# Performance work log

Hardware: AMD Instinct MI355X
Metric: run time of the kernel (lower is better)

Reference implementation:

```python
import jax, jax.numpy as jnp
import numpy as np

D_MODEL = 512
D_INNER = 2 * D_MODEL          # Mamba expand=2
D_STATE = 16                   # Mamba default d_state
D_CONV = 4                     # Mamba default d_conv
DT_RANK = D_MODEL // 16        # ceil(512/16) = 32
B, L = 2, 2048


def setup_inputs() -> dict:
    key = jax.random.key(0)
    ks = jax.random.split(key, 12)
    s = 0.02
    return {
        "query": jax.random.normal(ks[0], (B, L, D_MODEL), jnp.float32),
        "value": jax.random.normal(ks[1], (B, L, D_MODEL), jnp.float32),
        "diff_ts": jax.random.normal(ks[2], (B, D_MODEL), jnp.float32),
        # AdaLN modulation: SiLU -> Linear(D, 2D) (random instead of zero-init to exercise math)
        "ada_w": jax.random.normal(ks[3], (2 * D_MODEL, D_MODEL), jnp.float32) * s,
        "ada_b": jax.random.normal(ks[4], (2 * D_MODEL,), jnp.float32) * s,
        # Mamba params
        "in_proj_w": jax.random.normal(ks[5], (2 * D_INNER, D_MODEL), jnp.float32) * s,
        "conv_w": jax.random.normal(ks[6], (D_INNER, D_CONV), jnp.float32) * 0.1,
        "conv_b": jax.random.normal(ks[7], (D_INNER,), jnp.float32) * 0.1,
        "x_proj_w": jax.random.normal(ks[8], (DT_RANK + 2 * D_STATE, D_INNER), jnp.float32) * s,
        "dt_proj_w": jax.random.normal(ks[9], (D_INNER, DT_RANK), jnp.float32) * 0.1,
        "dt_proj_b": jax.random.normal(ks[10], (D_INNER,), jnp.float32) * 0.1,
        "A_log": jnp.broadcast_to(jnp.log(jnp.arange(1, D_STATE + 1, dtype=jnp.float32)), (D_INNER, D_STATE)) * jnp.ones((D_INNER, 1), jnp.float32),
        "D_param": jnp.ones((D_INNER,), jnp.float32),
        "out_proj_w": jax.random.normal(ks[11], (D_MODEL, D_INNER), jnp.float32) * s,
        "ln_g": jnp.ones((D_MODEL,), jnp.float32),
        "ln_b": jnp.zeros((D_MODEL,), jnp.float32),
    }


def reference(query, value, diff_ts, ada_w, ada_b, in_proj_w, conv_w, conv_b,
              x_proj_w, dt_proj_w, dt_proj_b, A_log, D_param, out_proj_w, ln_g, ln_b):
    silu = jax.nn.silu
    # ---- AdaLN modulation of query ----
    m = silu(diff_ts) @ ada_w.T + ada_b            # (B, 2D)
    scale, shift = jnp.split(m, 2, axis=-1)        # (B, D) each
    x = query * (1.0 + scale[:, None, :]) + shift[:, None, :]

    # ---- Mamba block ----
    xz = x @ in_proj_w.T                           # (B, L, 2*d_inner)
    xm, z = jnp.split(xz, 2, axis=-1)
    # causal depthwise conv1d (kernel D_CONV)
    xp = jnp.pad(xm, ((0, 0), (D_CONV - 1, 0), (0, 0)))
    Lq = xm.shape[1]
    xc = sum(xp[:, k:k + Lq, :] * conv_w[:, k] for k in range(D_CONV)) + conv_b
    xc = silu(xc)                                  # (B, L, d_inner)

    xdb = xc @ x_proj_w.T                          # (B, L, dt_rank + 2*N)
    dt = xdb[..., :DT_RANK]
    Bm = xdb[..., DT_RANK:DT_RANK + D_STATE]       # (B, L, N)
    Cm = xdb[..., DT_RANK + D_STATE:]              # (B, L, N)
    delta = jax.nn.softplus(dt @ dt_proj_w.T + dt_proj_b)  # (B, L, d_inner)
    A = -jnp.exp(A_log)                            # (d_inner, N)

    # ---- selective scan: h_t = exp(dt*A) h_{t-1} + dt*B_t*x_t ; y_t = C_t . h_t ----
    def step(h, inp):
        d_t, x_t, B_t, C_t = inp                   # (B,d), (B,d), (B,N), (B,N)
        dA = jnp.exp(d_t[..., None] * A)           # (B, d, N)
        h = dA * h + (d_t * x_t)[..., None] * B_t[:, None, :]
        y = jnp.einsum('bdn,bn->bd', h, C_t)
        return h, y

    seq = (delta.transpose(1, 0, 2), xc.transpose(1, 0, 2),
           Bm.transpose(1, 0, 2), Cm.transpose(1, 0, 2))
    h0 = jnp.zeros((query.shape[0], D_INNER, D_STATE), delta.dtype)
    _, ys = jax.lax.scan(step, h0, seq)            # (L, B, d_inner)

    y = ys.transpose(1, 0, 2) + xc * D_param
    y = y * silu(z)
    attn = y @ out_proj_w.T                        # (B, L, D)

    # ---- residual (dropout p=0) + LayerNorm ----
    out = query + attn
    mu = out.mean(-1, keepdims=True)
    var = out.var(-1, keepdims=True)
    return (out - mu) / jnp.sqrt(var + 1e-5) * ln_g + ln_b
```

## Files before the change

kernel.cpp:

```cpp
#include <hip/hip_runtime.h>
#include <hip/hip_bf16.h>

#define D_MODEL 512
#define D_INNER 1024
#define D_STATE 16
#define DT_RANK 32
#define BB 2
#define LL 2048
#define RR (BB*LL)
#define NC 128
#define CS 16

typedef __attribute__((ext_vector_type(8))) short short8;
typedef __attribute__((ext_vector_type(4))) short short4v;
typedef __attribute__((ext_vector_type(4))) float f32x4;

static __device__ __forceinline__ short f2bf(float f) {
  union { __hip_bfloat16 h; short s; } u;
  u.h = __float2bfloat16(f);
  return u.s;
}
static __device__ __forceinline__ float bfs2f(short s) {
  union { short s; __hip_bfloat16 h; } u;
  u.s = s;
  return __bfloat162float(u.h);
}

static __device__ __forceinline__ void gload16(const short* gp, short* lp) {
  __builtin_amdgcn_global_load_lds((const __attribute__((address_space(1))) short*)gp,
                                   (__attribute__((address_space(3))) short*)lp,
                                   16, 0, 0);
}

__global__ void k_ada_cvtw(const float* __restrict__ diff,
                           const float* __restrict__ aw,
                           const float* __restrict__ ab,
                           float* __restrict__ m,
                           const float* __restrict__ inw,
                           const float* __restrict__ outw,
                           const float* __restrict__ xw,
                           short* __restrict__ inwb,
                           short* __restrict__ outwb,
                           short* __restrict__ xwb) {
  const int bx = blockIdx.x;
  const int t = threadIdx.x;
  if (bx < 8) {
    __shared__ float sd[D_MODEL];
    const int b = bx >> 2;
    const int jb = bx & 3;
    for (int k = t; k < D_MODEL; k += 256) {
      float v = diff[b*D_MODEL + k];
      sd[k] = v / (1.f + __expf(-v));
    }
    __syncthreads();
    const int j = jb*256 + t;
    const float4* wr = reinterpret_cast<const float4*>(aw + (size_t)j*D_MODEL);
    float acc = ab[j];
    #pragma unroll 4
    for (int k4 = 0; k4 < D_MODEL/4; ++k4) {
      float4 wv = wr[k4];
      acc += sd[4*k4]*wv.x + sd[4*k4+1]*wv.y + sd[4*k4+2]*wv.z + sd[4*k4+3]*wv.w;
    }
    m[b*(2*D_MODEL) + j] = acc;
  } else {
    const int N1 = 2048*512, N2 = 512*1024, N3 = 64*1024;
    const int idx = ((bx - 8)*256 + t)*4;
    if (idx < N1) {
      float4 v = *reinterpret_cast<const float4*>(inw + idx);
      short4v s = {f2bf(v.x), f2bf(v.y), f2bf(v.z), f2bf(v.w)};
      *reinterpret_cast<short4v*>(inwb + idx) = s;
    } else if (idx < N1 + N2) {
      float4 v = *reinterpret_cast<const float4*>(outw + (idx - N1));
      short4v s = {f2bf(v.x), f2bf(v.y), f2bf(v.z), f2bf(v.w)};
      *reinterpret_cast<short4v*>(outwb + (idx - N1)) = s;
    } else if (idx < N1 + N2 + N3) {
      float4 v = *reinterpret_cast<const float4*>(xw + (idx - N1 - N2));
      short4v s = {f2bf(v.x), f2bf(v.y), f2bf(v.z), f2bf(v.w)};
      *reinterpret_cast<short4v*>(xwb + (idx - N1 - N2)) = s;
    }
  }
}

__global__ void k_amod(const float* __restrict__ q,
                       const float* __restrict__ m,
                       short* __restrict__ amod,
                       float* __restrict__ xdb) {
  const int bx = blockIdx.x;
  const int t = threadIdx.x;
  const int NB = (RR*D_MODEL)/(256*4);
  if (bx < NB) {
    const int idx = (bx*256 + t)*4;
    const int r = idx >> 9, k = idx & 511;
    const float* mrow = m + (r >> 11)*(2*D_MODEL);
    float4 a = *reinterpret_cast<const float4*>(q + idx);
    float4 s = *reinterpret_cast<const float4*>(mrow + k);
    float4 h = *reinterpret_cast<const float4*>(mrow + D_MODEL + k);
    short4v o = {f2bf(a.x*(1.f+s.x)+h.x), f2bf(a.y*(1.f+s.y)+h.y),
                 f2bf(a.z*(1.f+s.z)+h.z), f2bf(a.w*(1.f+s.w)+h.w)};
    *reinterpret_cast<short4v*>(amod + idx) = o;
  } else {
    const int idx = ((bx - NB)*256 + t)*4;
    *reinterpret_cast<float4*>(xdb + idx) = make_float4(0.f, 0.f, 0.f, 0.f);
  }
}

__global__ void __launch_bounds__(256) k_gemm_inproj(
    const short* __restrict__ A,
    const short* __restrict__ B,
    float* __restrict__ xm,
    short* __restrict__ zb) {
  __shared__ __align__(16) short As[128*64];
  __shared__ __align__(16) short Bs[128*64];
  const int t = threadIdx.x;
  const int w = t >> 6, lane = t & 63;
  const int quad = lane >> 4, l16 = lane & 15;
  const int row0 = blockIdx.y*128;
  const int col0 = blockIdx.x*128;
  const int K = D_MODEL;
  const int srow = w*8 + (lane >> 3);
  const int scol = (lane & 7)*8;
  const short* Ag = A + (size_t)(row0 + srow)*K + scol;
  const short* Bg = B + (size_t)(col0 + srow)*K + scol;
  short* AsW = As + w*512;
  short* BsW = Bs + w*512;
  const int ar0 = (w >> 1)*64;
  const int bc0 = (w & 1)*64;
  f32x4 acc[4][4] = {};
  for (int k0 = 0; k0 < K; k0 += 64) {
    #pragma unroll
    for (int i = 0; i < 4; ++i) {
      gload16(Ag + (size_t)(i*32)*K + k0, AsW + i*2048);
      gload16(Bg + (size_t)(i*32)*K + k0, BsW + i*2048);
    }
    __syncthreads();
    #pragma unroll
    for (int kk = 0; kk < 2; ++kk) {
      short8 af[4], bf[4];
      #pragma unroll
      for (int i = 0; i < 4; ++i)
        af[i] = *reinterpret_cast<const short8*>(&As[(ar0 + i*16 + l16)*64 + kk*32 + quad*8]);
      #pragma unroll
      for (int j = 0; j < 4; ++j)
        bf[j] = *reinterpret_cast<const short8*>(&Bs[(bc0 + j*16 + l16)*64 + kk*32 + quad*8]);
      #pragma unroll
      for (int i = 0; i < 4; ++i)
        #pragma unroll
        for (int j = 0; j < 4; ++j)
          acc[i][j] = __builtin_amdgcn_mfma_f32_16x16x32_bf16(af[i], bf[j], acc[i][j], 0, 0, 0);
    }
    __syncthreads();
  }
  const int orow = row0 + ar0 + quad*4;
  if (col0 < D_INNER) {
    #pragma unroll
    for (int i = 0; i < 4; ++i)
      #pragma unroll
      for (int j = 0; j < 4; ++j)
        #pragma unroll
        for (int r = 0; r < 4; ++r)
          xm[(size_t)(orow + i*16 + r)*D_INNER + col0 + bc0 + j*16 + l16] = acc[i][j][r];
  } else {
    const int zc0 = col0 - D_INNER + bc0;
    #pragma unroll
    for (int i = 0; i < 4; ++i)
      #pragma unroll
      for (int j = 0; j < 4; ++j)
        #pragma unroll
        for (int r = 0; r < 4; ++r)
          zb[(size_t)(orow + i*16 + r)*D_INNER + zc0 + j*16 + l16] = f2bf(acc[i][j][r]);
  }
}

__global__ void __launch_bounds__(256) k_gemm_out(
    const short* __restrict__ A,
    const short* __restrict__ B,
    float* __restrict__ C) {
  __shared__ __align__(16) short As[128*64];
  __shared__ __align__(16) short Bs[64*64];
  const int t = threadIdx.x;
  const int w = t >> 6, lane = t & 63;
  const int quad = lane >> 4, l16 = lane & 15;
  const int row0 = blockIdx.y*128;
  const int col0 = blockIdx.x*64;
  const int K = D_INNER;
  const int srow = w*8 + (lane >> 3);
  const int scol = (lane & 7)*8;
  const short* Ag = A + (size_t)(row0 + srow)*K + scol;
  const short* Bg = B + (size_t)(col0 + srow)*K + scol;
  short* AsW = As + w*512;
  short* BsW = Bs + w*512;
  f32x4 acc[2][4] = {};
  for (int k0 = 0; k0 < K; k0 += 64) {
    #pragma unroll
    for (int i = 0; i < 4; ++i)
      gload16(Ag + (size_t)(i*32)*K + k0, AsW + i*2048);
    #pragma unroll
    for (int i = 0; i < 2; ++i)
      gload16(Bg + (size_t)(i*32)*K + k0, BsW + i*2048);
    __syncthreads();
    #pragma unroll
    for (int kk = 0; kk < 2; ++kk) {
      short8 af[2], bf[4];
      #pragma unroll
      for (int i = 0; i < 2; ++i)
        af[i] = *reinterpret_cast<const short8*>(&As[(w*32 + i*16 + l16)*64 + kk*32 + quad*8]);
      #pragma unroll
      for (int j = 0; j < 4; ++j)
        bf[j] = *reinterpret_cast<const short8*>(&Bs[(j*16 + l16)*64 + kk*32 + quad*8]);
      #pragma unroll
      for (int i = 0; i < 2; ++i)
        #pragma unroll
        for (int j = 0; j < 4; ++j)
          acc[i][j] = __builtin_amdgcn_mfma_f32_16x16x32_bf16(af[i], bf[j], acc[i][j], 0, 0, 0);
    }
    __syncthreads();
  }
  #pragma unroll
  for (int i = 0; i < 2; ++i)
    #pragma unroll
    for (int j = 0; j < 4; ++j)
      #pragma unroll
      for (int r = 0; r < 4; ++r)
        C[(size_t)(row0 + w*32 + i*16 + quad*4 + r)*D_MODEL + col0 + j*16 + l16] = acc[i][j][r];
}

__global__ void __launch_bounds__(256) k_gemm_xproj(
    const short* __restrict__ A,
    const short* __restrict__ B,
    float* __restrict__ C) {
  __shared__ __align__(16) short As[128*64];
  __shared__ __align__(16) short Bs[64*64];
  const int t = threadIdx.x;
  const int w = t >> 6, lane = t & 63;
  const int quad = lane >> 4, l16 = lane & 15;
  const int row0 = blockIdx.y*128;
  const int kbase = blockIdx.x*(D_INNER/4);
  const int srow = w*8 + (lane >> 3);
  const int scol = (lane & 7)*8;
  const short* Ag = A + (size_t)(row0 + srow)*D_INNER + scol;
  const short* Bg = B + (size_t)srow*D_INNER + scol;
  short* AsW = As + w*512;
  short* BsW = Bs + w*512;
  f32x4 acc[2][4] = {};
  for (int k0 = kbase; k0 < kbase + D_INNER/4; k0 += 64) {
    #pragma unroll
    for (int i = 0; i < 4; ++i)
      gload16(Ag + (size_t)(i*32)*D_INNER + k0, AsW + i*2048);
    #pragma unroll
    for (int i = 0; i < 2; ++i)
      gload16(Bg + (size_t)(i*32)*D_INNER + k0, BsW + i*2048);
    __syncthreads();
    #pragma unroll
    for (int kk = 0; kk < 2; ++kk) {
      short8 af[2], bf[4];
      #pragma unroll
      for (int i = 0; i < 2; ++i)
        af[i] = *reinterpret_cast<const short8*>(&As[(w*32 + i*16 + l16)*64 + kk*32 + quad*8]);
      #pragma unroll
      for (int j = 0; j < 4; ++j)
        bf[j] = *reinterpret_cast<const short8*>(&Bs[(j*16 + l16)*64 + kk*32 + quad*8]);
      #pragma unroll
      for (int i = 0; i < 2; ++i)
        #pragma unroll
        for (int j = 0; j < 4; ++j)
          acc[i][j] = __builtin_amdgcn_mfma_f32_16x16x32_bf16(af[i], bf[j], acc[i][j], 0, 0, 0);
    }
    __syncthreads();
  }
  #pragma unroll
  for (int i = 0; i < 2; ++i)
    #pragma unroll
    for (int j = 0; j < 4; ++j)
      #pragma unroll
      for (int r = 0; r < 4; ++r)
        unsafeAtomicAdd(&C[(size_t)(row0 + w*32 + i*16 + quad*4 + r)*64 + j*16 + l16], acc[i][j][r]);
}

__global__ void k_conv4(const float* __restrict__ xm,
                        const float* __restrict__ cw,
                        const float* __restrict__ cb,
                        short* __restrict__ xcb) {
  const int gid = blockIdx.x*256 + threadIdx.x;
  const int d4 = (gid & 255)*4;
  const int r = gid >> 8;
  const int l = r & (LL-1);
  float4 w0 = *reinterpret_cast<const float4*>(cw + (size_t)(d4+0)*4);
  float4 w1 = *reinterpret_cast<const float4*>(cw + (size_t)(d4+1)*4);
  float4 w2 = *reinterpret_cast<const float4*>(cw + (size_t)(d4+2)*4);
  float4 w3 = *reinterpret_cast<const float4*>(cw + (size_t)(d4+3)*4);
  float4 res = *reinterpret_cast<const float4*>(cb + d4);
  #pragma unroll
  for (int k = 0; k < 4; ++k) {
    int ls = l + k - 3;
    if (ls >= 0) {
      float4 xv = *reinterpret_cast<const float4*>(xm + (size_t)(r + k - 3)*D_INNER + d4);
      float wk0 = (&w0.x)[k], wk1 = (&w1.x)[k], wk2 = (&w2.x)[k], wk3 = (&w3.x)[k];
      res.x += xv.x*wk0; res.y += xv.y*wk1; res.z += xv.z*wk2; res.w += xv.w*wk3;
    }
  }
  res.x = res.x / (1.f + __expf(-res.x));
  res.y = res.y / (1.f + __expf(-res.y));
  res.z = res.z / (1.f + __expf(-res.z));
  res.w = res.w / (1.f + __expf(-res.w));
  short4v rb = {f2bf(res.x), f2bf(res.y), f2bf(res.z), f2bf(res.w)};
  *reinterpret_cast<short4v*>(xcb + (size_t)r*D_INNER + d4) = rb;
}

__global__ void __launch_bounds__(256) k_dt(
    const float* __restrict__ xdb,
    const float* __restrict__ dtw,
    const float* __restrict__ dtb,
    float* __restrict__ dab) {
  const int lane = threadIdx.x & 63;
  const int w = threadIdx.x >> 6;
  const int d = blockIdx.x*64 + lane;
  const int r0 = (blockIdx.y*4 + w)*32;
  float wreg[DT_RANK];
  const float4* wp = reinterpret_cast<const float4*>(dtw + (size_t)d*DT_RANK);
  #pragma unroll
  for (int i = 0; i < 8; ++i) {
    float4 v = wp[i];
    wreg[4*i]=v.x; wreg[4*i+1]=v.y; wreg[4*i+2]=v.z; wreg[4*i+3]=v.w;
  }
  const float bv = dtb[d];
  #pragma unroll 4
  for (int rr = 0; rr < 32; ++rr) {
    const float* xr = xdb + (size_t)(r0+rr)*64;
    float a0 = 0.f, a1 = 0.f, a2 = 0.f, a3 = 0.f;
    #pragma unroll
    for (int i = 0; i < DT_RANK; i += 4) {
      a0 += xr[i]  *wreg[i];
      a1 += xr[i+1]*wreg[i+1];
      a2 += xr[i+2]*wreg[i+2];
      a3 += xr[i+3]*wreg[i+3];
    }
    dab[(size_t)(r0+rr)*D_INNER + d] = bv + ((a0+a1)+(a2+a3));
  }
}

static __device__ __forceinline__ void rpowers(float r, float* pw) {
  float p1 = r*r, p3 = p1*p1, p7 = p3*p3;
  pw[0]=r;      pw[1]=p1;     pw[2]=p1*r;    pw[3]=p3;
  pw[4]=p3*r;   pw[5]=p3*p1;  pw[6]=p3*pw[2];pw[7]=p7;
  pw[8]=p7*r;   pw[9]=p7*p1;  pw[10]=p7*pw[2];pw[11]=p7*p3;
  pw[12]=p7*pw[4];pw[13]=p7*pw[5];pw[14]=p7*pw[6];pw[15]=p7*p7;
}

__global__ void __launch_bounds__(256) k_scan1(
    const short* __restrict__ xcb,
    const float* __restrict__ xdb,
    const float* __restrict__ dab,
    float* __restrict__ rbuf,
    short* __restrict__ hstateb) {
  __shared__ float sx[CS*64];
  const int tid = threadIdx.x;
  const int d = blockIdx.x*256 + tid;
  const int c = blockIdx.y;
  const int b = blockIdx.z;
  const float* xrow = xdb + ((size_t)b*LL + (size_t)c*CS)*64;
  *reinterpret_cast<float4*>(&sx[tid*4]) = *reinterpret_cast<const float4*>(xrow + tid*4);
  const size_t base = ((size_t)b*LL + (size_t)c*CS)*D_INNER + d;
  float xvs[CS], dav[CS];
  #pragma unroll
  for (int t = 0; t < CS; ++t) {
    xvs[t] = bfs2f(xcb[base + (size_t)t*D_INNER]);
    dav[t] = dab[base + (size_t)t*D_INNER];
  }
  float h[D_STATE];
  #pragma unroll
  for (int n = 0; n < D_STATE; ++n) h[n] = 0.f;
  float rho = 1.f;
  __syncthreads();
  #pragma unroll
  for (int t = 0; t < CS; ++t) {
    float dacc = dav[t];
    float ex = __expf(dacc);
    float dlt = (dacc > 20.f) ? dacc : __logf(1.f + ex);
    float r = 1.f / (1.f + ex);
    rho *= r;
    float dx = dlt * xvs[t];
    float pw[D_STATE];
    rpowers(r, pw);
    #pragma unroll
    for (int j = 0; j < 4; ++j) {
      float4 Bv = *reinterpret_cast<const float4*>(&sx[t*64 + 32 + 4*j]);
      h[4*j]   = pw[4*j]  *h[4*j]   + dx*Bv.x;
      h[4*j+1] = pw[4*j+1]*h[4*j+1] + dx*Bv.y;
      h[4*j+2] = pw[4*j+2]*h[4*j+2] + dx*Bv.z;
      h[4*j+3] = pw[4*j+3]*h[4*j+3] + dx*Bv.w;
    }
  }
  const size_t s0 = (((size_t)b*NC + c)*D_INNER + d)*D_STATE;
  #pragma unroll
  for (int i = 0; i < 4; ++i) {
    short4v hv = {f2bf(h[4*i]), f2bf(h[4*i+1]), f2bf(h[4*i+2]), f2bf(h[4*i+3])};
    *reinterpret_cast<short4v*>(hstateb + s0 + 4*i) = hv;
  }
  rbuf[((size_t)b*NC + c)*D_INNER + d] = rho;
}

__global__ void __launch_bounds__(64) k_scan2(
    const float* __restrict__ rbuf,
    const short* __restrict__ hstateb,
    short* __restrict__ hpre) {
  const int gid = blockIdx.x*64 + threadIdx.x;
  const int b = gid >> 14;
  const int dn = gid & 16383;
  const int d = dn >> 4;
  const int n = dn & 15;
  const int p = n + 1;
  float h = 0.f;
  for (int cg = 0; cg < NC; cg += 16) {
    float rv[16], hl[16];
    #pragma unroll
    for (int i = 0; i < 16; ++i) {
      const int c = cg + i;
      rv[i] = rbuf[((size_t)b*NC + c)*D_INNER + d];
      hl[i] = bfs2f(hstateb[(((size_t)b*NC + c)*D_INNER + d)*D_STATE + n]);
    }
    #pragma unroll
    for (int i = 0; i < 16; ++i) {
      const int c = cg + i;
      float r = rv[i];
      float r2 = r*r, r4 = r2*r2, r8 = r4*r4;
      float a = (p & 1) ? r : 1.f;
      if (p & 2)  a *= r2;
      if (p & 4)  a *= r4;
      if (p & 8)  a *= r8;
      if (p & 16) a *= r8*r8;
      hpre[(((size_t)b*NC + c)*D_INNER + d)*D_STATE + n] = f2bf(h);
      h = a*h + hl[i];
    }
  }
}

__global__ void __launch_bounds__(256) k_scan3(
    const short* __restrict__ xcb,
    const float* __restrict__ xdb,
    const float* __restrict__ dab,
    const short* __restrict__ hpre,
    const float* __restrict__ Dp,
    const short* __restrict__ zb,
    short* __restrict__ y2b) {
  __shared__ float sx[CS*64];
  const int tid = threadIdx.x;
  const int d = blockIdx.x*256 + tid;
  const int c = blockIdx.y;
  const int b = blockIdx.z;
  const float* xrow = xdb + ((size_t)b*LL + (size_t)c*CS)*64;
  *reinterpret_cast<float4*>(&sx[tid*4]) = *reinterpret_cast<const float4*>(xrow + tid*4);
  const size_t base = ((size_t)b*LL + (size_t)c*CS)*D_INNER + d;
  float xvs[CS], dav[CS];
  #pragma unroll
  for (int t = 0; t < CS; ++t) {
    xvs[t] = bfs2f(xcb[base + (size_t)t*D_INNER]);
    dav[t] = dab[base + (size_t)t*D_INNER];
  }
  float h[D_STATE];
  const size_t s0 = (((size_t)b*NC + c)*D_INNER + d)*D_STATE;
  #pragma unroll
  for (int i = 0; i < 4; ++i) {
    short4v hv = *reinterpret_cast<const short4v*>(hpre + s0 + 4*i);
    h[4*i]   = bfs2f(hv.x);
    h[4*i+1] = bfs2f(hv.y);
    h[4*i+2] = bfs2f(hv.z);
    h[4*i+3] = bfs2f(hv.w);
  }
  const float dp = Dp[d];
  __syncthreads();
  #pragma unroll
  for (int t = 0; t < CS; ++t) {
    float dacc = dav[t];
    float ex = __expf(dacc);
    float dlt = (dacc > 20.f) ? dacc : __logf(1.f + ex);
    float r = 1.f / (1.f + ex);
    float dx = dlt * xvs[t];
    float pw[D_STATE];
    rpowers(r, pw);
    float y0 = 0.f, y1 = 0.f;
    #pragma unroll
    for (int j = 0; j < 4; ++j) {
      float4 Bv = *reinterpret_cast<const float4*>(&sx[t*64 + 32 + 4*j]);
      float4 Cv = *reinterpret_cast<const float4*>(&sx[t*64 + 48 + 4*j]);
      h[4*j]   = pw[4*j]  *h[4*j]   + dx*Bv.x;
      h[4*j+1] = pw[4*j+1]*h[4*j+1] + dx*Bv.y;
      h[4*j+2] = pw[4*j+2]*h[4*j+2] + dx*Bv.z;
      h[4*j+3] = pw[4*j+3]*h[4*j+3] + dx*Bv.w;
      y0 += h[4*j]  *Cv.x;
      y1 += h[4*j+1]*Cv.y;
      y0 += h[4*j+2]*Cv.z;
      y1 += h[4*j+3]*Cv.w;
    }
    float z = bfs2f(zb[base + (size_t)t*D_INNER]);
    float sz = z / (1.f + __expf(-z));
    y2b[base + (size_t)t*D_INNER] = f2bf(((y0+y1) + xvs[t]*dp) * sz);
  }
}

__global__ void k_ln(const float* __restrict__ attn,
                     const float* __restrict__ q,
                     const float* __restrict__ g,
                     const float* __restrict__ bb,
                     float* __restrict__ out) {
  const int r = blockIdx.x;
  const int t = threadIdx.x;
  float v0 = attn[(size_t)r*D_MODEL + t]       + q[(size_t)r*D_MODEL + t];
  float v1 = attn[(size_t)r*D_MODEL + 256 + t] + q[(size_t)r*D_MODEL + 256 + t];
  float s = v0 + v1, sq = v0*v0 + v1*v1;
  #pragma unroll
  for (int off = 32; off; off >>= 1) {
    s  += __shfl_xor(s, off);
    sq += __shfl_xor(sq, off);
  }
  __shared__ float ss[4], qq[4], stats[2];
  const int wid = t >> 6, lane = t & 63;
  if (lane == 0) { ss[wid] = s; qq[wid] = sq; }
  __syncthreads();
  if (t == 0) {
    float S = ss[0]+ss[1]+ss[2]+ss[3];
    float Q = qq[0]+qq[1]+qq[2]+qq[3];
    float mu = S * (1.f/D_MODEL);
    float var = Q * (1.f/D_MODEL) - mu*mu;
    stats[0] = mu; stats[1] = rsqrtf(var + 1e-5f);
  }
  __syncthreads();
  float mu = stats[0], rs = stats[1];
  out[(size_t)r*D_MODEL + t]       = (v0-mu)*rs*g[t]     + bb[t];
  out[(size_t)r*D_MODEL + 256 + t] = (v1-mu)*rs*g[256+t] + bb[256+t];
}

extern "C" void kernel_launch(void* const* d_in, const int* in_sizes, int n_in,
                              void* d_out, int out_size, void* d_ws, size_t ws_size,
                              hipStream_t stream) {
  (void)in_sizes; (void)n_in; (void)out_size; (void)ws_size;
  const float* q    = (const float*)d_in[0];
  const float* diff = (const float*)d_in[2];
  const float* aw   = (const float*)d_in[3];
  const float* ab   = (const float*)d_in[4];
  const float* inw  = (const float*)d_in[5];
  const float* cw   = (const float*)d_in[6];
  const float* cb   = (const float*)d_in[7];
  const float* xw   = (const float*)d_in[8];
  const float* dtw  = (const float*)d_in[9];
  const float* dtb  = (const float*)d_in[10];
  const float* Dp   = (const float*)d_in[12];
  const float* outw = (const float*)d_in[13];
  const float* lng  = (const float*)d_in[14];
  const float* lnb  = (const float*)d_in[15];
  float* out = (float*)d_out;

  float* ws = (float*)d_ws;
  float* m      = ws;
  float* xm     = ws + 2048;
  float* xdb    = xm + (size_t)RR*D_INNER;
  float* rbuf   = xdb + (size_t)RR*64;
  float* attn2  = rbuf + (size_t)BB*NC*D_INNER;
  float* dab    = attn2 + (size_t)RR*D_MODEL;
  short* amod    = (short*)(dab + (size_t)RR*D_INNER);
  short* inwb    = amod + (size_t)RR*D_MODEL;
  short* outwb   = inwb + (size_t)2*D_INNER*D_MODEL;
  short* xwb     = outwb + (size_t)D_MODEL*D_INNER;
  short* y2b     = xwb + (size_t)64*D_INNER;
  short* xcb     = y2b + (size_t)RR*D_INNER;
  short* zb      = xcb + (size_t)RR*D_INNER;
  short* hstateb = zb + (size_t)RR*D_INNER;
  short* hpre    = hstateb + (size_t)BB*NC*D_INNER*D_STATE;

  const int cvtBlocks = (2048*512 + 512*1024 + 64*1024)/(256*4);
  k_ada_cvtw<<<8 + cvtBlocks, 256, 0, stream>>>(
      diff, aw, ab, m, inw, outw, xw, inwb, outwb, xwb);
  k_amod<<<(RR*D_MODEL)/(256*4) + (RR*64)/(256*4), 256, 0, stream>>>(q, m, amod, xdb);
  k_gemm_inproj<<<dim3((2*D_INNER)/128, RR/128), 256, 0, stream>>>(amod, inwb, xm, zb);
  k_conv4<<<(RR*D_INNER/4)/256, 256, 0, stream>>>(xm, cw, cb, xcb);
  k_gemm_xproj<<<dim3(4, RR/128), 256, 0, stream>>>(xcb, xwb, xdb);
  k_dt<<<dim3(16, 32), 256, 0, stream>>>(xdb, dtw, dtb, dab);
  k_scan1<<<dim3(D_INNER/256, NC, BB), 256, 0, stream>>>(xcb, xdb, dab, rbuf, hstateb);
  k_scan2<<<(BB*D_INNER*16)/64, 64, 0, stream>>>(rbuf, hstateb, hpre);
  k_scan3<<<dim3(D_INNER/256, NC, BB), 256, 0, stream>>>(xcb, xdb, dab, hpre, Dp, zb, y2b);
  k_gemm_out<<<dim3(D_MODEL/64, RR/128), 256, 0, stream>>>(y2b, outwb, attn2);
  k_ln<<<RR, 256, 0, stream>>>(attn2, q, lng, lnb, out);
}
```

Baseline: 249.0 us.

## Store in_proj x half in bf16 and precompute softplus decay terms in k_dt

The x half of the in_proj output is now written as bf16 instead of fp32, which halves that intermediate's write and the conv kernel's read. The softplus, exp-decay ratio and dt*x product are computed once in k_dt and stored as two fp32 buffers, so both scan passes no longer repeat the transcendental math. In exchange, k_scan1 and k_scan3 read two fp32 arrays instead of one fp32 plus one bf16, adding memory traffic. Storing x in bf16 before the convolution also adds rounding error.

```diff
diff --git a/kernel.cpp b/kernel.cpp
--- a/kernel.cpp
+++ b/kernel.cpp
@@ -107,7 +107,7 @@
 __global__ void __launch_bounds__(256) k_gemm_inproj(
     const short* __restrict__ A,
     const short* __restrict__ B,
-    float* __restrict__ xm,
+    short* __restrict__ xmb,
     short* __restrict__ zb) {
   __shared__ __align__(16) short As[128*64];
   __shared__ __align__(16) short Bs[128*64];
@@ -158,7 +158,7 @@
       for (int j = 0; j < 4; ++j)
         #pragma unroll
         for (int r = 0; r < 4; ++r)
-          xm[(size_t)(orow + i*16 + r)*D_INNER + col0 + bc0 + j*16 + l16] = acc[i][j][r];
+          xmb[(size_t)(orow + i*16 + r)*D_INNER + col0 + bc0 + j*16 + l16] = f2bf(acc[i][j][r]);
   } else {
     const int zc0 = col0 - D_INNER + bc0;
     #pragma unroll
@@ -276,7 +276,7 @@
         unsafeAtomicAdd(&C[(size_t)(row0 + w*32 + i*16 + quad*4 + r)*64 + j*16 + l16], acc[i][j][r]);
 }
 
-__global__ void k_conv4(const float* __restrict__ xm,
+__global__ void k_conv4(const short* __restrict__ xmb,
                         const float* __restrict__ cw,
                         const float* __restrict__ cb,
                         short* __restrict__ xcb) {
@@ -293,9 +293,10 @@
   for (int k = 0; k < 4; ++k) {
     int ls = l + k - 3;
     if (ls >= 0) {
-      float4 xv = *reinterpret_cast<const float4*>(xm + (size_t)(r + k - 3)*D_INNER + d4);
+      short4v xv = *reinterpret_cast<const short4v*>(xmb + (size_t)(r + k - 3)*D_INNER + d4);
       float wk0 = (&w0.x)[k], wk1 = (&w1.x)[k], wk2 = (&w2.x)[k], wk3 = (&w3.x)[k];
-      res.x += xv.x*wk0; res.y += xv.y*wk1; res.z += xv.z*wk2; res.w += xv.w*wk3;
+      res.x += bfs2f(xv.x)*wk0; res.y += bfs2f(xv.y)*wk1;
+      res.z += bfs2f(xv.z)*wk2; res.w += bfs2f(xv.w)*wk3;
     }
   }
   res.x = res.x / (1.f + __expf(-res.x));
@@ -310,7 +311,9 @@
     const float* __restrict__ xdb,
     const float* __restrict__ dtw,
     const float* __restrict__ dtb,
-    float* __restrict__ dab) {
+    const short* __restrict__ xcb,
+    float* __restrict__ rf,
+    float* __restrict__ dxf) {
   const int lane = threadIdx.x & 63;
   const int w = threadIdx.x >> 6;
   const int d = blockIdx.x*64 + lane;
@@ -334,7 +337,13 @@
       a2 += xr[i+2]*wreg[i+2];
       a3 += xr[i+3]*wreg[i+3];
     }
-    dab[(size_t)(r0+rr)*D_INNER + d] = bv + ((a0+a1)+(a2+a3));
+    float dacc = bv + ((a0+a1)+(a2+a3));
+    float ex = __expf(dacc);
+    float dlt = (dacc > 20.f) ? dacc : __logf(1.f + ex);
+    float r = 1.f / (1.f + ex);
+    float xv = bfs2f(xcb[(size_t)(r0+rr)*D_INNER + d]);
+    rf[(size_t)(r0+rr)*D_INNER + d]  = r;
+    dxf[(size_t)(r0+rr)*D_INNER + d] = dlt * xv;
   }
 }
 
@@ -347,9 +356,9 @@
 }
 
 __global__ void __launch_bounds__(256) k_scan1(
-    const short* __restrict__ xcb,
+    const float* __restrict__ rf,
+    const float* __restrict__ dxf,
     const float* __restrict__ xdb,
-    const float* __restrict__ dab,
     float* __restrict__ rbuf,
     short* __restrict__ hstateb) {
   __shared__ float sx[CS*64];
@@ -360,11 +369,11 @@
   const float* xrow = xdb + ((size_t)b*LL + (size_t)c*CS)*64;
   *reinterpret_cast<float4*>(&sx[tid*4]) = *reinterpret_cast<const float4*>(xrow + tid*4);
   const size_t base = ((size_t)b*LL + (size_t)c*CS)*D_INNER + d;
-  float xvs[CS], dav[CS];
+  float rv[CS], dxv[CS];
   #pragma unroll
   for (int t = 0; t < CS; ++t) {
-    xvs[t] = bfs2f(xcb[base + (size_t)t*D_INNER]);
-    dav[t] = dab[base + (size_t)t*D_INNER];
+    rv[t]  = rf[base + (size_t)t*D_INNER];
+    dxv[t] = dxf[base + (size_t)t*D_INNER];
   }
   float h[D_STATE];
   #pragma unroll
@@ -373,12 +382,9 @@
   __syncthreads();
   #pragma unroll
   for (int t = 0; t < CS; ++t) {
-    float dacc = dav[t];
-    float ex = __expf(dacc);
-    float dlt = (dacc > 20.f) ? dacc : __logf(1.f + ex);
-    float r = 1.f / (1.f + ex);
+    float r = rv[t];
     rho *= r;
-    float dx = dlt * xvs[t];
+    float dx = dxv[t];
     float pw[D_STATE];
     rpowers(r, pw);
     #pragma unroll
@@ -435,9 +441,10 @@
 }
 
 __global__ void __launch_bounds__(256) k_scan3(
+    const float* __restrict__ rf,
+    const float* __restrict__ dxf,
     const short* __restrict__ xcb,
     const float* __restrict__ xdb,
-    const float* __restrict__ dab,
     const short* __restrict__ hpre,
     const float* __restrict__ Dp,
     const short* __restrict__ zb,
@@ -450,11 +457,12 @@
   const float* xrow = xdb + ((size_t)b*LL + (size_t)c*CS)*64;
   *reinterpret_cast<float4*>(&sx[tid*4]) = *reinterpret_cast<const float4*>(xrow + tid*4);
   const size_t base = ((size_t)b*LL + (size_t)c*CS)*D_INNER + d;
-  float xvs[CS], dav[CS];
+  float rv[CS], dxv[CS], xvs[CS];
   #pragma unroll
   for (int t = 0; t < CS; ++t) {
+    rv[t]  = rf[base + (size_t)t*D_INNER];
+    dxv[t] = dxf[base + (size_t)t*D_INNER];
     xvs[t] = bfs2f(xcb[base + (size_t)t*D_INNER]);
-    dav[t] = dab[base + (size_t)t*D_INNER];
   }
   float h[D_STATE];
   const size_t s0 = (((size_t)b*NC + c)*D_INNER + d)*D_STATE;
@@ -470,11 +478,8 @@
   __syncthreads();
   #pragma unroll
   for (int t = 0; t < CS; ++t) {
-    float dacc = dav[t];
-    float ex = __expf(dacc);
-    float dlt = (dacc > 20.f) ? dacc : __logf(1.f + ex);
-    float r = 1.f / (1.f + ex);
-    float dx = dlt * xvs[t];
+    float r = rv[t];
+    float dx = dxv[t];
     float pw[D_STATE];
     rpowers(r, pw);
     float y0 = 0.f, y1 = 0.f;
@@ -551,32 +556,33 @@
 
   float* ws = (float*)d_ws;
   float* m      = ws;
-  float* xm     = ws + 2048;
-  float* xdb    = xm + (size_t)RR*D_INNER;
+  float* xdb    = ws + 2048;
   float* rbuf   = xdb + (size_t)RR*64;
   float* attn2  = rbuf + (size_t)BB*NC*D_INNER;
-  float* dab    = attn2 + (size_t)RR*D_MODEL;
-  short* amod    = (short*)(dab + (size_t)RR*D_INNER);
+  float* rf     = attn2 + (size_t)RR*D_MODEL;
+  float* dxf    = rf + (size_t)RR*D_INNER;
+  short* amod    = (short*)(dxf + (size_t)RR*D_INNER);
   short* inwb    = amod + (size_t)RR*D_MODEL;
   short* outwb   = inwb + (size_t)2*D_INNER*D_MODEL;
   short* xwb     = outwb + (size_t)D_MODEL*D_INNER;
   short* y2b     = xwb + (size_t)64*D_INNER;
   short* xcb     = y2b + (size_t)RR*D_INNER;
   short* zb      = xcb + (size_t)RR*D_INNER;
-  short* hstateb = zb + (size_t)RR*D_INNER;
+  short* xmb     = zb + (size_t)RR*D_INNER;
+  short* hstateb = xmb + (size_t)RR*D_INNER;
   short* hpre    = hstateb + (size_t)BB*NC*D_INNER*D_STATE;
 
   const int cvtBlocks = (2048*512 + 512*1024 + 64*1024)/(256*4);
   k_ada_cvtw<<<8 + cvtBlocks, 256, 0, stream>>>(
       diff, aw, ab, m, inw, outw, xw, inwb, outwb, xwb);
   k_amod<<<(RR*D_MODEL)/(256*4) + (RR*64)/(256*4), 256, 0, stream>>>(q, m, amod, xdb);
-  k_gemm_inproj<<<dim3((2*D_INNER)/128, RR/128), 256, 0, stream>>>(amod, inwb, xm, zb);
-  k_conv4<<<(RR*D_INNER/4)/256, 256, 0, stream>>>(xm, cw, cb, xcb);
+  k_gemm_inproj<<<dim3((2*D_INNER)/128, RR/128), 256, 0, stream>>>(amod, inwb, xmb, zb);
+  k_conv4<<<(RR*D_INNER/4)/256, 256, 0, stream>>>(xmb, cw, cb, xcb);
   k_gemm_xproj<<<dim3(4, RR/128), 256, 0, stream>>>(xcb, xwb, xdb);
-  k_dt<<<dim3(16, 32), 256, 0, stream>>>(xdb, dtw, dtb, dab);
-  k_scan1<<<dim3(D_INNER/256, NC, BB), 256, 0, stream>>>(xcb, xdb, dab, rbuf, hstateb);
+  k_dt<<<dim3(16, 32), 256, 0, stream>>>(xdb, dtw, dtb, xcb, rf, dxf);
+  k_scan1<<<dim3(D_INNER/256, NC, BB), 256, 0, stream>>>(rf, dxf, xdb, rbuf, hstateb);
   k_scan2<<<(BB*D_INNER*16)/64, 64, 0, stream>>>(rbuf, hstateb, hpre);
-  k_scan3<<<dim3(D_INNER/256, NC, BB), 256, 0, stream>>>(xcb, xdb, dab, hpre, Dp, zb, y2b);
+  k_scan3<<<dim3(D_INNER/256, NC, BB), 256, 0, stream>>>(rf, dxf, xcb, xdb, hpre, Dp, zb, y2b);
   k_gemm_out<<<dim3(D_MODEL/64, RR/128), 256, 0, stream>>>(y2b, outwb, attn2);
   k_ln<<<RR, 256, 0, stream>>>(attn2, q, lng, lnb, out);
 }
```

After: 265.1 us. 1.06x slower.
